# Performance work log

Measured on AMD Instinct MI355X. Metric: run time of the kernel, lower is better.

Reference implementation:

```python
import jax, jax.numpy as jnp
import numpy as np

N_TOKENS = 16384
HIDDEN = 4096
N_EXPERTS = 64
TOP_K = 8


def setup_inputs() -> dict:
    key = jax.random.key(0)
    kx, kw, kb = jax.random.split(key, 3)
    x = jax.random.normal(kx, (N_TOKENS, HIDDEN), dtype=jnp.float32)
    # nn.Linear(hidden_dim, expert_num): weight [E, H], bias [E]
    W = jax.random.normal(kw, (N_EXPERTS, HIDDEN), dtype=jnp.float32) * (1.0 / np.sqrt(HIDDEN))
    b = jax.random.normal(kb, (N_EXPERTS,), dtype=jnp.float32) * 0.01
    return {"x": x, "W": W, "b": b}


def reference(x, W, b):
    # gate linear: [N, H] @ [H, E] + [E] -> [N, E]
    router = jnp.einsum("nh,eh->ne", x, W) + b
    # softmax over experts
    router_logits = jax.nn.softmax(router, axis=-1)
    # top-k over experts: values/indices [N, K]
    top_k_logits, top_k_indices = jax.lax.top_k(router_logits, TOP_K)
    # renormalize the selected probs
    router_weight = top_k_logits / jnp.sum(top_k_logits, axis=-1, keepdims=True)
    router_weight = router_weight.astype(x.dtype)
    # one-hot mask [N, K, E] -> permute(2,1,0) -> [E, K, N]
    expert_mask = jax.nn.one_hot(top_k_indices, N_EXPERTS, dtype=jnp.int32)
    expert_mask = jnp.transpose(expert_mask, (2, 1, 0))
    return (router, router_weight, top_k_indices, expert_mask)
```

## Files before the change

### kernel.cpp

```cpp
#include <hip/hip_runtime.h>

#define N_TOK 16384
#define HID   4096
#define N_EXP 64
#define TOPK  8

#define SPLIT  4
#define KSLICE (HID / SPLIT)
#define CH     32
#define NCH    (KSLICE / CH)
#define LSTR   68

#define OFF_WT   (N_TOK * N_EXP)
#define OFF_IDX  (OFF_WT + N_TOK * TOPK)
#define OFF_MASK (OFF_IDX + N_TOK * TOPK)

__global__ __launch_bounds__(256, 4)
void router_gemm(const float* __restrict__ x, const float* __restrict__ W,
                 float* __restrict__ router)
{
    __shared__ float xs[2][CH][LSTR];
    __shared__ float ws[2][CH][LSTR];

    const int tid = threadIdx.x;
    const int tb  = blockIdx.x & 255;
    const int ks  = blockIdx.x >> 8;
    const long t0 = (long)tb * 64;
    const int h0  = ks * KSLICE;

    const int lane = tid & 63;
    const int wv   = tid >> 6;
    const int eg   = lane & 15;
    const int tg   = lane >> 4;
    const int trow = wv * 16 + tg * 4;
    const int ecol = eg * 4;

    const int tf = tid >> 3;
    const int hq = tid & 7;

    const float* xsrc = x + (t0 + tf) * (long)HID + h0 + 4 * hq;
    const float* wsrc = W + (long)tf * HID + h0 + 4 * hq;

    float acc[4][4] = {{0.f}};

    float4 px0 = *(const float4*)(xsrc);
    float4 px1 = *(const float4*)(xsrc + 32 * (long)HID);
    float4 pw0 = *(const float4*)(wsrc);
    float4 pw1 = *(const float4*)(wsrc + 32 * (long)HID);

#pragma unroll
    for (int j = 0; j < 4; ++j) {
        xs[0][4 * hq + j][tf]      = ((const float*)&px0)[j];
        xs[0][4 * hq + j][tf + 32] = ((const float*)&px1)[j];
        ws[0][4 * hq + j][tf]      = ((const float*)&pw0)[j];
        ws[0][4 * hq + j][tf + 32] = ((const float*)&pw1)[j];
    }
    __syncthreads();

    for (int c = 0; c < NCH; ++c) {
        const int buf = c & 1;

        if (c + 1 < NCH) {
            const float* xn = xsrc + (c + 1) * CH;
            const float* wn = wsrc + (c + 1) * CH;
            px0 = *(const float4*)(xn);
            px1 = *(const float4*)(xn + 32 * (long)HID);
            pw0 = *(const float4*)(wn);
            pw1 = *(const float4*)(wn + 32 * (long)HID);
        }

#pragma unroll 4
        for (int k = 0; k < CH; ++k) {
            float4 xq = *(const float4*)&xs[buf][k][trow];
            float4 wq = *(const float4*)&ws[buf][k][ecol];
            acc[0][0] = fmaf(xq.x, wq.x, acc[0][0]);
            acc[0][1] = fmaf(xq.x, wq.y, acc[0][1]);
            acc[0][2] = fmaf(xq.x, wq.z, acc[0][2]);
            acc[0][3] = fmaf(xq.x, wq.w, acc[0][3]);
            acc[1][0] = fmaf(xq.y, wq.x, acc[1][0]);
            acc[1][1] = fmaf(xq.y, wq.y, acc[1][1]);
            acc[1][2] = fmaf(xq.y, wq.z, acc[1][2]);
            acc[1][3] = fmaf(xq.y, wq.w, acc[1][3]);
            acc[2][0] = fmaf(xq.z, wq.x, acc[2][0]);
            acc[2][1] = fmaf(xq.z, wq.y, acc[2][1]);
            acc[2][2] = fmaf(xq.z, wq.z, acc[2][2]);
            acc[2][3] = fmaf(xq.z, wq.w, acc[2][3]);
            acc[3][0] = fmaf(xq.w, wq.x, acc[3][0]);
            acc[3][1] = fmaf(xq.w, wq.y, acc[3][1]);
            acc[3][2] = fmaf(xq.w, wq.z, acc[3][2]);
            acc[3][3] = fmaf(xq.w, wq.w, acc[3][3]);
        }

        if (c + 1 < NCH) {
            const int nb = buf ^ 1;
#pragma unroll
            for (int j = 0; j < 4; ++j) {
                xs[nb][4 * hq + j][tf]      = ((const float*)&px0)[j];
                xs[nb][4 * hq + j][tf + 32] = ((const float*)&px1)[j];
                ws[nb][4 * hq + j][tf]      = ((const float*)&pw0)[j];
                ws[nb][4 * hq + j][tf + 32] = ((const float*)&pw1)[j];
            }
        }
        __syncthreads();
    }

    float* rbase = router + (t0 + trow) * (long)N_EXP + ecol;
#pragma unroll
    for (int i = 0; i < 4; ++i)
#pragma unroll
        for (int j = 0; j < 4; ++j)
            unsafeAtomicAdd(rbase + (long)i * N_EXP + j, acc[i][j]);
}

__global__ __launch_bounds__(256)
void router_topk(float* __restrict__ router, const float* __restrict__ b,
                 float* __restrict__ out)
{
    const int tid  = threadIdx.x;
    const int lane = tid & 63;
    const int wv   = tid >> 6;
    const int n    = blockIdx.x * 4 + wv;

    float l = router[(long)n * N_EXP + lane] + b[lane];
    router[(long)n * N_EXP + lane] = l;

    float m = l;
#pragma unroll
    for (int o = 32; o > 0; o >>= 1) m = fmaxf(m, __shfl_xor(m, o));
    float p = expf(l - m);
    float Z = p;
#pragma unroll
    for (int o = 32; o > 0; o >>= 1) Z += __shfl_xor(Z, o);
    float prob = p / Z;

    float cur = prob;
    float myv = 0.f;
    int   myi = 0;
    float ssum = 0.f;
#pragma unroll
    for (int k = 0; k < TOPK; ++k) {
        float v = cur;
        int   id = lane;
#pragma unroll
        for (int o = 32; o > 0; o >>= 1) {
            float ov = __shfl_xor(v, o);
            int   oi = __shfl_xor(id, o);
            if (ov > v || (ov == v && oi < id)) { v = ov; id = oi; }
        }
        if (lane == k)  { myv = v; myi = id; }
        if (lane == id) cur = -1.f;
        ssum += v;
    }

    if (lane < TOPK) {
        out[OFF_WT  + (long)n * TOPK + lane] = myv / ssum;
        out[OFF_IDX + (long)n * TOPK + lane] = (float)myi;
        out[OFF_MASK + (long)myi * (TOPK * N_TOK) + (long)lane * N_TOK + n] = 1.0f;
    }
}

extern "C" void kernel_launch(void* const* d_in, const int* in_sizes, int n_in,
                              void* d_out, int out_size, void* d_ws, size_t ws_size,
                              hipStream_t stream)
{
    const float* x = (const float*)d_in[0];
    const float* W = (const float*)d_in[1];
    const float* b = (const float*)d_in[2];
    float* out = (float*)d_out;

    hipMemsetAsync(out, 0, (size_t)out_size * sizeof(float), stream);

    hipLaunchKernelGGL(router_gemm, dim3(256 * SPLIT), dim3(256), 0, stream,
                       x, W, out);
    hipLaunchKernelGGL(router_topk, dim3(N_TOK / 4), dim3(256), 0, stream,
                       out, b, out);
}
```

Before: 455.4 us.

## Double token tile per block and write expert mask densely in separate kernel

The GEMM block now covers 128 tokens instead of 64, so each thread accumulates 8x4 outputs and each W tile in shared memory is reused across twice as many rows. This cuts redundant W traffic and halves the grid, at the cost of more registers and lower occupancy (launch bounds lowered to 2). The full-output memset is shrunk to the router region only. The expert mask is now written by a new kernel that emits dense float4 zeros and ones, replacing the scattered single-element writes over a fully zeroed buffer.

```diff
diff --git a/kernel.cpp b/kernel.cpp
--- a/kernel.cpp
+++ b/kernel.cpp
@@ -9,31 +9,31 @@
 #define KSLICE (HID / SPLIT)
 #define CH     32
 #define NCH    (KSLICE / CH)
-#define LSTR   68
+#define TB     128
+#define XSTR   132
+#define WSTR   68
 
 #define OFF_WT   (N_TOK * N_EXP)
 #define OFF_IDX  (OFF_WT + N_TOK * TOPK)
 #define OFF_MASK (OFF_IDX + N_TOK * TOPK)
 
-__global__ __launch_bounds__(256, 4)
+__global__ __launch_bounds__(256, 2)
 void router_gemm(const float* __restrict__ x, const float* __restrict__ W,
                  float* __restrict__ router)
 {
-    __shared__ float xs[2][CH][LSTR];
-    __shared__ float ws[2][CH][LSTR];
+    __shared__ __align__(16) float xs[2][CH][XSTR];
+    __shared__ __align__(16) float ws[2][CH][WSTR];
 
     const int tid = threadIdx.x;
-    const int tb  = blockIdx.x & 255;
-    const int ks  = blockIdx.x >> 8;
-    const long t0 = (long)tb * 64;
+    const int tb  = blockIdx.x & 127;
+    const int ks  = blockIdx.x >> 7;
+    const long t0 = (long)tb * TB;
     const int h0  = ks * KSLICE;
 
     const int lane = tid & 63;
     const int wv   = tid >> 6;
-    const int eg   = lane & 15;
-    const int tg   = lane >> 4;
-    const int trow = wv * 16 + tg * 4;
-    const int ecol = eg * 4;
+    const int trow = wv * 16 + (lane >> 4) * 4;
+    const int ecol = (lane & 15) * 4;
 
     const int tf = tid >> 3;
     const int hq = tid & 7;
@@ -41,19 +41,20 @@
     const float* xsrc = x + (t0 + tf) * (long)HID + h0 + 4 * hq;
     const float* wsrc = W + (long)tf * HID + h0 + 4 * hq;
 
-    float acc[4][4] = {{0.f}};
-
-    float4 px0 = *(const float4*)(xsrc);
-    float4 px1 = *(const float4*)(xsrc + 32 * (long)HID);
-    float4 pw0 = *(const float4*)(wsrc);
-    float4 pw1 = *(const float4*)(wsrc + 32 * (long)HID);
-
-#pragma unroll
-    for (int j = 0; j < 4; ++j) {
-        xs[0][4 * hq + j][tf]      = ((const float*)&px0)[j];
-        xs[0][4 * hq + j][tf + 32] = ((const float*)&px1)[j];
-        ws[0][4 * hq + j][tf]      = ((const float*)&pw0)[j];
-        ws[0][4 * hq + j][tf + 32] = ((const float*)&pw1)[j];
+    float acc[8][4] = {{0.f}};
+    float4 px[4], pw[2];
+
+#pragma unroll
+    for (int j = 0; j < 4; ++j) px[j] = *(const float4*)(xsrc + (long)(32 * j) * HID);
+#pragma unroll
+    for (int j = 0; j < 2; ++j) pw[j] = *(const float4*)(wsrc + (long)(32 * j) * HID);
+
+#pragma unroll
+    for (int jj = 0; jj < 4; ++jj) {
+#pragma unroll
+        for (int j = 0; j < 4; ++j) xs[0][4 * hq + jj][tf + 32 * j] = ((const float*)&px[j])[jj];
+#pragma unroll
+        for (int j = 0; j < 2; ++j) ws[0][4 * hq + jj][tf + 32 * j] = ((const float*)&pw[j])[jj];
     }
     __syncthreads();
 
@@ -61,55 +62,57 @@
         const int buf = c & 1;
 
         if (c + 1 < NCH) {
-            const float* xn = xsrc + (c + 1) * CH;
-            const float* wn = wsrc + (c + 1) * CH;
-            px0 = *(const float4*)(xn);
-            px1 = *(const float4*)(xn + 32 * (long)HID);
-            pw0 = *(const float4*)(wn);
-            pw1 = *(const float4*)(wn + 32 * (long)HID);
+#pragma unroll
+            for (int j = 0; j < 4; ++j) px[j] = *(const float4*)(xsrc + (c + 1) * CH + (long)(32 * j) * HID);
+#pragma unroll
+            for (int j = 0; j < 2; ++j) pw[j] = *(const float4*)(wsrc + (c + 1) * CH + (long)(32 * j) * HID);
         }
 
 #pragma unroll 4
         for (int k = 0; k < CH; ++k) {
-            float4 xq = *(const float4*)&xs[buf][k][trow];
+            float4 xa = *(const float4*)&xs[buf][k][trow];
+            float4 xb = *(const float4*)&xs[buf][k][trow + 64];
             float4 wq = *(const float4*)&ws[buf][k][ecol];
-            acc[0][0] = fmaf(xq.x, wq.x, acc[0][0]);
-            acc[0][1] = fmaf(xq.x, wq.y, acc[0][1]);
-            acc[0][2] = fmaf(xq.x, wq.z, acc[0][2]);
-            acc[0][3] = fmaf(xq.x, wq.w, acc[0][3]);
-            acc[1][0] = fmaf(xq.y, wq.x, acc[1][0]);
-            acc[1][1] = fmaf(xq.y, wq.y, acc[1][1]);
-            acc[1][2] = fmaf(xq.y, wq.z, acc[1][2]);
-            acc[1][3] = fmaf(xq.y, wq.w, acc[1][3]);
-            acc[2][0] = fmaf(xq.z, wq.x, acc[2][0]);
-            acc[2][1] = fmaf(xq.z, wq.y, acc[2][1]);
-            acc[2][2] = fmaf(xq.z, wq.z, acc[2][2]);
-            acc[2][3] = fmaf(xq.z, wq.w, acc[2][3]);
-            acc[3][0] = fmaf(xq.w, wq.x, acc[3][0]);
-            acc[3][1] = fmaf(xq.w, wq.y, acc[3][1]);
-            acc[3][2] = fmaf(xq.w, wq.z, acc[3][2]);
-            acc[3][3] = fmaf(xq.w, wq.w, acc[3][3]);
+#pragma unroll
+            for (int i = 0; i < 4; ++i) {
+                float xv = ((const float*)&xa)[i];
+                acc[i][0] = fmaf(xv, wq.x, acc[i][0]);
+                acc[i][1] = fmaf(xv, wq.y, acc[i][1]);
+                acc[i][2] = fmaf(xv, wq.z, acc[i][2]);
+                acc[i][3] = fmaf(xv, wq.w, acc[i][3]);
+            }
+#pragma unroll
+            for (int i = 0; i < 4; ++i) {
+                float xv = ((const float*)&xb)[i];
+                acc[4 + i][0] = fmaf(xv, wq.x, acc[4 + i][0]);
+                acc[4 + i][1] = fmaf(xv, wq.y, acc[4 + i][1]);
+                acc[4 + i][2] = fmaf(xv, wq.z, acc[4 + i][2]);
+                acc[4 + i][3] = fmaf(xv, wq.w, acc[4 + i][3]);
+            }
         }
 
         if (c + 1 < NCH) {
             const int nb = buf ^ 1;
 #pragma unroll
-            for (int j = 0; j < 4; ++j) {
-                xs[nb][4 * hq + j][tf]      = ((const float*)&px0)[j];
-                xs[nb][4 * hq + j][tf + 32] = ((const float*)&px1)[j];
-                ws[nb][4 * hq + j][tf]      = ((const float*)&pw0)[j];
-                ws[nb][4 * hq + j][tf + 32] = ((const float*)&pw1)[j];
+            for (int jj = 0; jj < 4; ++jj) {
+#pragma unroll
+                for (int j = 0; j < 4; ++j) xs[nb][4 * hq + jj][tf + 32 * j] = ((const float*)&px[j])[jj];
+#pragma unroll
+                for (int j = 0; j < 2; ++j) ws[nb][4 * hq + jj][tf + 32 * j] = ((const float*)&pw[j])[jj];
             }
         }
         __syncthreads();
     }
 
-    float* rbase = router + (t0 + trow) * (long)N_EXP + ecol;
-#pragma unroll
-    for (int i = 0; i < 4; ++i)
-#pragma unroll
-        for (int j = 0; j < 4; ++j)
-            unsafeAtomicAdd(rbase + (long)i * N_EXP + j, acc[i][j]);
+#pragma unroll
+    for (int h = 0; h < 2; ++h) {
+        float* rbase = router + (t0 + trow + 64 * h) * (long)N_EXP + ecol;
+#pragma unroll
+        for (int i = 0; i < 4; ++i)
+#pragma unroll
+            for (int j = 0; j < 4; ++j)
+                unsafeAtomicAdd(rbase + (long)i * N_EXP + j, acc[4 * h + i][j]);
+    }
 }
 
 __global__ __launch_bounds__(256)
@@ -155,7 +158,28 @@
     if (lane < TOPK) {
         out[OFF_WT  + (long)n * TOPK + lane] = myv / ssum;
         out[OFF_IDX + (long)n * TOPK + lane] = (float)myi;
-        out[OFF_MASK + (long)myi * (TOPK * N_TOK) + (long)lane * N_TOK + n] = 1.0f;
+    }
+}
+
+__global__ __launch_bounds__(256)
+void mask_fill(const float* __restrict__ idxf, float* __restrict__ mask)
+{
+    const int k  = blockIdx.x >> 4;
+    const int n0 = ((blockIdx.x & 15) * 256 + threadIdx.x) * 4;
+
+    int sel[4];
+#pragma unroll
+    for (int t = 0; t < 4; ++t)
+        sel[t] = (int)idxf[(long)(n0 + t) * TOPK + k];
+
+#pragma unroll 8
+    for (int e = 0; e < N_EXP; ++e) {
+        float4 v;
+        v.x = (sel[0] == e) ? 1.0f : 0.0f;
+        v.y = (sel[1] == e) ? 1.0f : 0.0f;
+        v.z = (sel[2] == e) ? 1.0f : 0.0f;
+        v.w = (sel[3] == e) ? 1.0f : 0.0f;
+        *(float4*)(mask + (long)(e * TOPK + k) * N_TOK + n0) = v;
     }
 }
 
@@ -168,10 +192,12 @@
     const float* b = (const float*)d_in[2];
     float* out = (float*)d_out;
 
-    hipMemsetAsync(out, 0, (size_t)out_size * sizeof(float), stream);
-
-    hipLaunchKernelGGL(router_gemm, dim3(256 * SPLIT), dim3(256), 0, stream,
+    hipMemsetAsync(out, 0, (size_t)(N_TOK * N_EXP) * sizeof(float), stream);
+
+    hipLaunchKernelGGL(router_gemm, dim3(TB * SPLIT == 512 ? 512 : 512), dim3(256), 0, stream,
                        x, W, out);
     hipLaunchKernelGGL(router_topk, dim3(N_TOK / 4), dim3(256), 0, stream,
                        out, b, out);
-}
+    hipLaunchKernelGGL(mask_fill, dim3(128), dim3(256), 0, stream,
+                       out + OFF_IDX, out + OFF_MASK);
+}
```

Measured after the change: 475.7 us. +4.5%, slower.
